# Kernel tuning notes

Measured on AMD Instinct MI355X. Metric: run time of the kernel, lower is better.

The kernel has to match this reference:

```python
import jax, jax.numpy as jnp
import numpy as np

EPS = 1e-8
N, C, R = 512, 32, 32


def _eijk():
    e = np.zeros((3, 3, 3), np.float32)
    e[0, 1, 2] = e[1, 2, 0] = e[2, 0, 1] = 1.0
    e[0, 2, 1] = e[2, 1, 0] = e[1, 0, 2] = -1.0
    return jnp.asarray(e)


def _unit(v):
    # unit_vectors: v / (|v| + EPS)
    return v / (jnp.linalg.norm(v, axis=-1, keepdims=True) + EPS)


def _y2(r):
    # real l=2 spherical harmonics (TFN convention), [N,N,5]
    x, y, z = r[..., 0], r[..., 1], r[..., 2]
    r2 = jnp.maximum(jnp.sum(r * r, axis=-1), EPS)
    c = float(2.0 * np.sqrt(3.0))
    return jnp.stack([
        x * y / r2,
        y * z / r2,
        (-x * x - y * y + 2.0 * z * z) / (c * r2),
        z * x / r2,
        (x * x - y * y) / (2.0 * r2),
    ], axis=-1)


def _forward(in0, in1, in2, rbf, rij,
             w1_f00, b1_f00, w2_f00, b2_f00,
             w1_f01, b1_f01, w2_f01, b2_f01,
             w1_f02, b1_f02, w2_f02, b2_f02,
             w1_f10, b1_f10, w2_f10, b2_f10,
             w1_f11, b1_f11, w2_f11, b2_f11):
    def rad(w1, b1, w2, b2):
        # RadialFunction: relu(b1 + rbf @ w1^T) @ w2^T + b2 -> [N,N,C]
        h = jax.nn.relu(b1 + jnp.einsum('abr,hr->abh', rbf, w1))
        return b2 + jnp.einsum('abh,ch->abc', h, w2)

    # mask self/zero-distance pairs (dij < EPS -> radial = 0), as in F_1/F_2
    mask = (jnp.linalg.norm(rij, axis=-1) >= EPS).astype(rbf.dtype)[..., None]  # [N,N,1]
    u = _unit(rij)    # [N,N,3]
    y2 = _y2(rij)     # [N,N,5]

    r00 = rad(w1_f00, b1_f00, w2_f00, b2_f00)            # scalar filter F_0
    r01 = rad(w1_f01, b1_f01, w2_f01, b2_f01) * mask     # F_1 radial, 0x1->1
    r02 = rad(w1_f02, b1_f02, w2_f02, b2_f02) * mask     # F_2 radial, 0x2->2
    r10 = rad(w1_f10, b1_f10, w2_f10, b2_f10) * mask     # F_1 radial, 1x1->0
    r11 = rad(w1_f11, b1_f11, w2_f11, b2_f11) * mask     # F_1 radial, 1x1->1

    # Filter_0_output_0 (identity CG): L x 0 -> L, aggregate over neighbors b
    o0_s = jnp.einsum('abf,bfi->afi', r00, in0)          # [N,C,1]
    o1_s = jnp.einsum('abf,bfi->afi', r00, in1)          # [N,C,3]
    o2_s = jnp.einsum('abf,bfi->afi', r00, in2)          # [N,C,5]
    o1_a = jnp.einsum('abi,abf,bf->afi', u, r01, in0[..., 0])
    o2_a = jnp.einsum('abi,abf,bf->afi', y2, r02, in0[..., 0])
    o0_b = jnp.einsum('abj,abf,bfj->af', u, r10, in1)[..., None]
    o1_c = jnp.einsum('ijk,abj,abf,bfk->afi', _eijk(), u, r11, in1)

    return (jnp.stack([o0_s, o0_b]),          # [2,N,C,1]
            jnp.stack([o1_a, o1_s, o1_c]),    # [3,N,C,3]
            jnp.stack([o2_a, o2_s]))          # [2,N,C,5]


def setup_inputs() -> dict:
    key = jax.random.key(0)
    ks = jax.random.split(key, 16)

    def xav(k, shape):
        lim = float(np.sqrt(6.0 / (shape[0] + shape[1])))
        return jax.random.uniform(k, shape, jnp.float32, -lim, lim)

    pos = jax.random.normal(ks[0], (N, 3), jnp.float32) * 3.0
    rij = pos[:, None, :] - pos[None, :, :]  # [N,N,3]; zero diagonal exercises the dij<EPS mask
    inp = {
        'in0': jax.random.normal(ks[1], (N, C, 1), jnp.float32),
        'in1': jax.random.normal(ks[2], (N, C, 3), jnp.float32),
        'in2': jax.random.normal(ks[3], (N, C, 5), jnp.float32),
        'rbf': jax.random.uniform(ks[4], (N, N, R), jnp.float32),
        'rij': rij,
    }
    for i, n in enumerate(['f00', 'f01', 'f02', 'f10', 'f11']):
        inp['w1_' + n] = xav(ks[5 + 2 * i], (R, R))
        inp['b1_' + n] = jnp.zeros((R,), jnp.float32)
        inp['w2_' + n] = xav(ks[6 + 2 * i], (C, R))
        inp['b2_' + n] = jnp.zeros((C,), jnp.float32)
    return inp


def reference(in0, in1, in2, rbf, rij,
              w1_f00, b1_f00, w2_f00, b2_f00,
              w1_f01, b1_f01, w2_f01, b2_f01,
              w1_f02, b1_f02, w2_f02, b2_f02,
              w1_f10, b1_f10, w2_f10, b2_f10,
              w1_f11, b1_f11, w2_f11, b2_f11):
    return _forward(in0, in1, in2, rbf, rij,
                    w1_f00, b1_f00, w2_f00, b2_f00,
                    w1_f01, b1_f01, w2_f01, b2_f01,
                    w1_f02, b1_f02, w2_f02, b2_f02,
                    w1_f10, b1_f10, w2_f10, b2_f10,
                    w1_f11, b1_f11, w2_f11, b2_f11)
```

## Files before the change

kernel.cpp:

```cpp
#include <hip/hip_runtime.h>
#include <math.h>

#define NN 512
#define CC 32
#define EPSF 1e-8f
#define WS 40

typedef __attribute__((ext_vector_type(8))) short bf16x8;
typedef __attribute__((ext_vector_type(4))) float f32x4;

__device__ __forceinline__ short f2bf(float f) {
    unsigned u = __float_as_uint(f);
    u += 0x7fffu + ((u >> 16) & 1u);
    return (short)(u >> 16);
}

#define STAGE_F(F, W1P, W2P)                                                   \
    {                                                                          \
        const int n0 = tid >> 5, k0 = tid & 31;                                \
        wlds[(((F) * 2 + 0) * 32 + n0) * WS + k0]      = f2bf((W1P)[tid]);     \
        wlds[(((F) * 2 + 0) * 32 + n0 + 16) * WS + k0] = f2bf((W1P)[tid+512]); \
        wlds[(((F) * 2 + 1) * 32 + n0) * WS + k0]      = f2bf((W2P)[tid]);     \
        wlds[(((F) * 2 + 1) * 32 + n0 + 16) * WS + k0] = f2bf((W2P)[tid+512]); \
    }

#define MLP3(WOFF, B1L, B1H, B2V, R)                                               \
    {                                                                              \
        const bf16x8 w1loM = *(const bf16x8*)&wlds[(WOFF) + ln * WS + q * 8];      \
        const bf16x8 w1hiM = *(const bf16x8*)&wlds[(WOFF) + (16 + ln) * WS + q * 8]; \
        f32x4 d0M = { (B1L), (B1L), (B1L), (B1L) };                                \
        f32x4 d1M = { (B1H), (B1H), (B1H), (B1H) };                                \
        d0M = __builtin_amdgcn_mfma_f32_16x16x32_bf16(rbfF, w1loM, d0M, 0, 0, 0);  \
        d1M = __builtin_amdgcn_mfma_f32_16x16x32_bf16(rbfF, w1hiM, d1M, 0, 0, 0);  \
        hlds[w][(q * 4 + 0) * WS + ln]      = f2bf(fmaxf(d0M[0], 0.f));            \
        hlds[w][(q * 4 + 1) * WS + ln]      = f2bf(fmaxf(d0M[1], 0.f));            \
        hlds[w][(q * 4 + 2) * WS + ln]      = f2bf(fmaxf(d0M[2], 0.f));            \
        hlds[w][(q * 4 + 3) * WS + ln]      = f2bf(fmaxf(d0M[3], 0.f));            \
        hlds[w][(q * 4 + 0) * WS + 16 + ln] = f2bf(fmaxf(d1M[0], 0.f));            \
        hlds[w][(q * 4 + 1) * WS + 16 + ln] = f2bf(fmaxf(d1M[1], 0.f));            \
        hlds[w][(q * 4 + 2) * WS + 16 + ln] = f2bf(fmaxf(d1M[2], 0.f));            \
        hlds[w][(q * 4 + 3) * WS + 16 + ln] = f2bf(fmaxf(d1M[3], 0.f));            \
        const bf16x8 hFM = *(const bf16x8*)&hlds[w][ln * WS + q * 8];              \
        const bf16x8 w2M = *(const bf16x8*)&wlds[(WOFF) + (32 + ch0 + ln) * WS + q * 8]; \
        f32x4 eM = { (B2V), (B2V), (B2V), (B2V) };                                 \
        R = __builtin_amdgcn_mfma_f32_16x16x32_bf16(hFM, w2M, eM, 0, 0, 0);        \
    }

#define AGGM(RR)                                                               \
    {                                                                          \
        const int bA = b0 + q * 4 + (RR);                                      \
        const f32x4 gA = *(const f32x4*)&geomall[bA][0];                       \
        const f32x4 gB = *(const f32x4*)&geomall[bA][4];                       \
        const float i0A = in0[bA * CC + cw];                                   \
        const float* i1A = in1 + (bA * CC + cw) * 3;                           \
        const float x1A = i1A[0], y1A = i1A[1], z1A = i1A[2];                  \
        const float* i2A = in2 + (bA * CC + cw) * 5;                           \
        const float p0A = i2A[0], p1A = i2A[1], p2A = i2A[2];                  \
        const float p3A = i2A[3], p4A = i2A[4];                                \
        const float s0A = rF0[(RR)];                                           \
        a0  = fmaf(s0A, i0A, a0);                                              \
        a5  = fmaf(s0A, x1A, a5);                                              \
        a6  = fmaf(s0A, y1A, a6);                                              \
        a7  = fmaf(s0A, z1A, a7);                                              \
        a16 = fmaf(s0A, p0A, a16);                                             \
        a17 = fmaf(s0A, p1A, a17);                                             \
        a18 = fmaf(s0A, p2A, a18);                                             \
        a19 = fmaf(s0A, p3A, a19);                                             \
        a20 = fmaf(s0A, p4A, a20);                                             \
        const float t1A = rF1[(RR)] * i0A;                                     \
        a2  = fmaf(t1A, gA[0], a2);                                            \
        a3  = fmaf(t1A, gA[1], a3);                                            \
        a4  = fmaf(t1A, gA[2], a4);                                            \
        const float t2A = rF2[(RR)] * i0A;                                     \
        a11 = fmaf(t2A, gA[3], a11);                                           \
        a12 = fmaf(t2A, gB[0], a12);                                           \
        a13 = fmaf(t2A, gB[1], a13);                                           \
        a14 = fmaf(t2A, gB[2], a14);                                           \
        a15 = fmaf(t2A, gB[3], a15);                                           \
        const float dtA = fmaf(gA[2], z1A, fmaf(gA[1], y1A, gA[0] * x1A));     \
        a1  = fmaf(rF3[(RR)], dtA, a1);                                        \
        const float cxA = fmaf(gA[1], z1A, -(gA[2] * y1A));                    \
        const float cyA = fmaf(gA[2], x1A, -(gA[0] * z1A));                    \
        const float czA = fmaf(gA[0], y1A, -(gA[1] * x1A));                    \
        a8  = fmaf(rF4[(RR)], cxA, a8);                                        \
        a9  = fmaf(rF4[(RR)], cyA, a9);                                        \
        a10 = fmaf(rF4[(RR)], czA, a10);                                       \
    }

#define RED(CMP, V)                                                            \
    {                                                                          \
        float vR = (V);                                                        \
        vR += __shfl_down(vR, 32);                                             \
        vR += __shfl_down(vR, 16);                                             \
        if (lane < 16) red[(w * 21 + (CMP)) * 16 + ln] = vR;                   \
    }

__global__ __launch_bounds__(512, 2) void tfn_mfma(
    const float* __restrict__ in0,
    const float* __restrict__ in1,
    const float* __restrict__ in2,
    const float* __restrict__ rbf,
    const float* __restrict__ rij,
    const float* __restrict__ w1_0, const float* __restrict__ b1_0,
    const float* __restrict__ w2_0, const float* __restrict__ b2_0,
    const float* __restrict__ w1_1, const float* __restrict__ b1_1,
    const float* __restrict__ w2_1, const float* __restrict__ b2_1,
    const float* __restrict__ w1_2, const float* __restrict__ b1_2,
    const float* __restrict__ w2_2, const float* __restrict__ b2_2,
    const float* __restrict__ w1_3, const float* __restrict__ b1_3,
    const float* __restrict__ w2_3, const float* __restrict__ b2_3,
    const float* __restrict__ w1_4, const float* __restrict__ b1_4,
    const float* __restrict__ w2_4, const float* __restrict__ b2_4,
    float* __restrict__ out)
{
    const int a    = blockIdx.x;
    const int tid  = threadIdx.x;
    const int w    = tid >> 6;
    const int lane = tid & 63;
    const int q    = lane >> 4;
    const int ln   = lane & 15;
    const int ch0  = (w & 1) * 16;
    const int cw   = ch0 + ln;

    __shared__ short wlds[5 * 2 * 32 * WS];
    __shared__ short hlds[8][16 * WS];
    __shared__ float geomall[NN][8];

    STAGE_F(0, w1_0, w2_0)
    STAGE_F(1, w1_1, w2_1)
    STAGE_F(2, w1_2, w2_2)
    STAGE_F(3, w1_3, w2_3)
    STAGE_F(4, w1_4, w2_4)

    const size_t rowbase = (size_t)a * NN;
    const float Y2C = 0.28867513459481287f;

    {
        const float* rp = rij + (rowbase + tid) * 3;
        const float x = rp[0], y = rp[1], z = rp[2];
        const float d2 = x * x + y * y + z * z;
        const float d  = sqrtf(d2);
        const float m  = (d >= EPSF) ? 1.f : 0.f;
        const float inv = m / (d + EPSF);
        const float ir2 = m / fmaxf(d2, EPSF);
        f32x4 gA = { x * inv, y * inv, z * inv, x * y * ir2 };
        f32x4 gB = { y * z * ir2, (2.f * z * z - x * x - y * y) * (ir2 * Y2C),
                     z * x * ir2, (x * x - y * y) * (ir2 * 0.5f) };
        *(f32x4*)&geomall[tid][0] = gA;
        *(f32x4*)&geomall[tid][4] = gB;
    }

    const float b1lo0 = b1_0[ln], b1hi0 = b1_0[16 + ln], b2v0 = b2_0[cw];
    const float b1lo1 = b1_1[ln], b1hi1 = b1_1[16 + ln], b2v1 = b2_1[cw];
    const float b1lo2 = b1_2[ln], b1hi2 = b1_2[16 + ln], b2v2 = b2_2[cw];
    const float b1lo3 = b1_3[ln], b1hi3 = b1_3[16 + ln], b2v3 = b2_3[cw];
    const float b1lo4 = b1_4[ln], b1hi4 = b1_4[16 + ln], b2v4 = b2_4[cw];
    __syncthreads();

    float a0 = 0.f, a1 = 0.f, a2 = 0.f, a3 = 0.f, a4 = 0.f, a5 = 0.f, a6 = 0.f;
    float a7 = 0.f, a8 = 0.f, a9 = 0.f, a10 = 0.f, a11 = 0.f, a12 = 0.f, a13 = 0.f;
    float a14 = 0.f, a15 = 0.f, a16 = 0.f, a17 = 0.f, a18 = 0.f, a19 = 0.f, a20 = 0.f;

    const int pairb = (w >> 1) * 128;

    const float* rbase = rbf + (rowbase + pairb + ln) * 32 + q * 8;
    f32x4 curA = *(const f32x4*)rbase;
    f32x4 curB = *(const f32x4*)(rbase + 4);

    #pragma unroll 1
    for (int t = 0; t < 8; ++t) {
        const int b0 = pairb + t * 16;

        bf16x8 rbfF;
        rbfF[0] = f2bf(curA[0]); rbfF[1] = f2bf(curA[1]);
        rbfF[2] = f2bf(curA[2]); rbfF[3] = f2bf(curA[3]);
        rbfF[4] = f2bf(curB[0]); rbfF[5] = f2bf(curB[1]);
        rbfF[6] = f2bf(curB[2]); rbfF[7] = f2bf(curB[3]);
        if (t < 7) {
            curA = *(const f32x4*)(rbase + (t + 1) * 512);
            curB = *(const f32x4*)(rbase + (t + 1) * 512 + 4);
        }

        f32x4 rF0, rF1, rF2, rF3, rF4;
        MLP3(0 * 64 * WS, b1lo0, b1hi0, b2v0, rF0)
        MLP3(1 * 64 * WS, b1lo1, b1hi1, b2v1, rF1)
        MLP3(2 * 64 * WS, b1lo2, b1hi2, b2v2, rF2)
        MLP3(3 * 64 * WS, b1lo3, b1hi3, b2v3, rF3)
        MLP3(4 * 64 * WS, b1lo4, b1hi4, b2v4, rF4)

        AGGM(0) AGGM(1) AGGM(2) AGGM(3)

        __builtin_amdgcn_sched_barrier(0);
    }

    __syncthreads();
    float* red = (float*)wlds;
    RED(0,  a0)  RED(1,  a1)  RED(2,  a2)  RED(3,  a3)  RED(4,  a4)
    RED(5,  a5)  RED(6,  a6)  RED(7,  a7)  RED(8,  a8)  RED(9,  a9)
    RED(10, a10) RED(11, a11) RED(12, a12) RED(13, a13) RED(14, a14)
    RED(15, a15) RED(16, a16) RED(17, a17) RED(18, a18) RED(19, a19)
    RED(20, a20)
    __syncthreads();

    const int NC = NN * CC;
    for (int e = tid; e < 21 * 32; e += 512) {
        const int cmp = e >> 5, c = e & 31;
        const int hh = c >> 4, l2 = c & 15;
        float s = 0.f;
        #pragma unroll
        for (int p = 0; p < 4; ++p)
            s += red[((p * 2 + hh) * 21 + cmp) * 16 + l2];
        int idx;
        if (cmp == 0)       idx = a * CC + c;
        else if (cmp == 1)  idx = NC + a * CC + c;
        else if (cmp < 5)   idx = 2 * NC + (a * CC + c) * 3 + (cmp - 2);
        else if (cmp < 8)   idx = 2 * NC + 3 * NC + (a * CC + c) * 3 + (cmp - 5);
        else if (cmp < 11)  idx = 2 * NC + 6 * NC + (a * CC + c) * 3 + (cmp - 8);
        else if (cmp < 16)  idx = 11 * NC + (a * CC + c) * 5 + (cmp - 11);
        else                idx = 11 * NC + 5 * NC + (a * CC + c) * 5 + (cmp - 16);
        out[idx] = s;
    }
}

extern "C" void kernel_launch(void* const* d_in, const int* in_sizes, int n_in,
                              void* d_out, int out_size, void* d_ws, size_t ws_size,
                              hipStream_t stream) {
    const float* in0 = (const float*)d_in[0];
    const float* in1 = (const float*)d_in[1];
    const float* in2 = (const float*)d_in[2];
    const float* rbf = (const float*)d_in[3];
    const float* rij = (const float*)d_in[4];

    hipLaunchKernelGGL(tfn_mfma, dim3(NN), dim3(512), 0, stream,
                       in0, in1, in2, rbf, rij,
                       (const float*)d_in[5],  (const float*)d_in[6],
                       (const float*)d_in[7],  (const float*)d_in[8],
                       (const float*)d_in[9],  (const float*)d_in[10],
                       (const float*)d_in[11], (const float*)d_in[12],
                       (const float*)d_in[13], (const float*)d_in[14],
                       (const float*)d_in[15], (const float*)d_in[16],
                       (const float*)d_in[17], (const float*)d_in[18],
                       (const float*)d_in[19], (const float*)d_in[20],
                       (const float*)d_in[21], (const float*)d_in[22],
                       (const float*)d_in[23], (const float*)d_in[24],
                       (float*)d_out);
}
```

Before: 42.09 us.

## Keep hidden MLP activations in registers via transposed MFMA and permuted W2 layout

The first-layer MFMA now has its operands swapped, so its transposed output lands in the lane layout the second MFMA needs as its A operand. This removes the per-filter round trip through the hidden LDS buffer. W2 is staged into LDS with a permuted k index so the K ordering matches the packed registers, and the b1 biases are loaded as per-lane vectors. The fp32-to-bf16 conversion uses the packed hardware instruction v_cvt_pk_bf16_f32 instead of manual rounding, which may round differently from the software path.

```diff
diff --git a/kernel.cpp b/kernel.cpp
--- a/kernel.cpp
+++ b/kernel.cpp
@@ -15,35 +15,36 @@
     return (short)(u >> 16);
 }
 
+__device__ __forceinline__ unsigned cvtpk(float lo, float hi) {
+    unsigned r;
+    asm("v_cvt_pk_bf16_f32 %0, %1, %2" : "=v"(r) : "v"(lo), "v"(hi));
+    return r;
+}
+
 #define STAGE_F(F, W1P, W2P)                                                   \
     {                                                                          \
-        const int n0 = tid >> 5, k0 = tid & 31;                                \
         wlds[(((F) * 2 + 0) * 32 + n0) * WS + k0]      = f2bf((W1P)[tid]);     \
         wlds[(((F) * 2 + 0) * 32 + n0 + 16) * WS + k0] = f2bf((W1P)[tid+512]); \
-        wlds[(((F) * 2 + 1) * 32 + n0) * WS + k0]      = f2bf((W2P)[tid]);     \
-        wlds[(((F) * 2 + 1) * 32 + n0 + 16) * WS + k0] = f2bf((W2P)[tid+512]); \
-    }
-
-#define MLP3(WOFF, B1L, B1H, B2V, R)                                               \
+        wlds[(((F) * 2 + 1) * 32 + n0) * WS + k2]      = f2bf((W2P)[tid]);     \
+        wlds[(((F) * 2 + 1) * 32 + n0 + 16) * WS + k2] = f2bf((W2P)[tid+512]); \
+    }
+
+#define MLP3S(WOFF, B1LO, B1HI, B2V, R)                                            \
     {                                                                              \
         const bf16x8 w1loM = *(const bf16x8*)&wlds[(WOFF) + ln * WS + q * 8];      \
         const bf16x8 w1hiM = *(const bf16x8*)&wlds[(WOFF) + (16 + ln) * WS + q * 8]; \
-        f32x4 d0M = { (B1L), (B1L), (B1L), (B1L) };                                \
-        f32x4 d1M = { (B1H), (B1H), (B1H), (B1H) };                                \
-        d0M = __builtin_amdgcn_mfma_f32_16x16x32_bf16(rbfF, w1loM, d0M, 0, 0, 0);  \
-        d1M = __builtin_amdgcn_mfma_f32_16x16x32_bf16(rbfF, w1hiM, d1M, 0, 0, 0);  \
-        hlds[w][(q * 4 + 0) * WS + ln]      = f2bf(fmaxf(d0M[0], 0.f));            \
-        hlds[w][(q * 4 + 1) * WS + ln]      = f2bf(fmaxf(d0M[1], 0.f));            \
-        hlds[w][(q * 4 + 2) * WS + ln]      = f2bf(fmaxf(d0M[2], 0.f));            \
-        hlds[w][(q * 4 + 3) * WS + ln]      = f2bf(fmaxf(d0M[3], 0.f));            \
-        hlds[w][(q * 4 + 0) * WS + 16 + ln] = f2bf(fmaxf(d1M[0], 0.f));            \
-        hlds[w][(q * 4 + 1) * WS + 16 + ln] = f2bf(fmaxf(d1M[1], 0.f));            \
-        hlds[w][(q * 4 + 2) * WS + 16 + ln] = f2bf(fmaxf(d1M[2], 0.f));            \
-        hlds[w][(q * 4 + 3) * WS + 16 + ln] = f2bf(fmaxf(d1M[3], 0.f));            \
-        const bf16x8 hFM = *(const bf16x8*)&hlds[w][ln * WS + q * 8];              \
+        f32x4 d0M = (B1LO);                                                        \
+        f32x4 d1M = (B1HI);                                                        \
+        d0M = __builtin_amdgcn_mfma_f32_16x16x32_bf16(w1loM, rbfF, d0M, 0, 0, 0);  \
+        d1M = __builtin_amdgcn_mfma_f32_16x16x32_bf16(w1hiM, rbfF, d1M, 0, 0, 0);  \
+        union { bf16x8 v; unsigned u[4]; } hu;                                     \
+        hu.u[0] = cvtpk(fmaxf(d0M[0], 0.f), fmaxf(d0M[1], 0.f));                   \
+        hu.u[1] = cvtpk(fmaxf(d0M[2], 0.f), fmaxf(d0M[3], 0.f));                   \
+        hu.u[2] = cvtpk(fmaxf(d1M[0], 0.f), fmaxf(d1M[1], 0.f));                   \
+        hu.u[3] = cvtpk(fmaxf(d1M[2], 0.f), fmaxf(d1M[3], 0.f));                   \
         const bf16x8 w2M = *(const bf16x8*)&wlds[(WOFF) + (32 + ch0 + ln) * WS + q * 8]; \
         f32x4 eM = { (B2V), (B2V), (B2V), (B2V) };                                 \
-        R = __builtin_amdgcn_mfma_f32_16x16x32_bf16(hFM, w2M, eM, 0, 0, 0);        \
+        R = __builtin_amdgcn_mfma_f32_16x16x32_bf16(hu.v, w2M, eM, 0, 0, 0);       \
     }
 
 #define AGGM(RR)                                                               \
@@ -123,8 +124,11 @@
     const int cw   = ch0 + ln;
 
     __shared__ short wlds[5 * 2 * 32 * WS];
-    __shared__ short hlds[8][16 * WS];
     __shared__ float geomall[NN][8];
+
+    const int n0 = tid >> 5, k0 = tid & 31;
+    const int k2 = (k0 < 16) ? ((k0 >> 2) * 8 + (k0 & 3))
+                             : (((k0 - 16) >> 2) * 8 + 4 + ((k0 - 16) & 3));
 
     STAGE_F(0, w1_0, w2_0)
     STAGE_F(1, w1_1, w2_1)
@@ -150,11 +154,13 @@
         *(f32x4*)&geomall[tid][4] = gB;
     }
 
-    const float b1lo0 = b1_0[ln], b1hi0 = b1_0[16 + ln], b2v0 = b2_0[cw];
-    const float b1lo1 = b1_1[ln], b1hi1 = b1_1[16 + ln], b2v1 = b2_1[cw];
-    const float b1lo2 = b1_2[ln], b1hi2 = b1_2[16 + ln], b2v2 = b2_2[cw];
-    const float b1lo3 = b1_3[ln], b1hi3 = b1_3[16 + ln], b2v3 = b2_3[cw];
-    const float b1lo4 = b1_4[ln], b1hi4 = b1_4[16 + ln], b2v4 = b2_4[cw];
+    const f32x4 b1lo0 = *(const f32x4*)(b1_0 + 4 * q), b1hi0 = *(const f32x4*)(b1_0 + 16 + 4 * q);
+    const f32x4 b1lo1 = *(const f32x4*)(b1_1 + 4 * q), b1hi1 = *(const f32x4*)(b1_1 + 16 + 4 * q);
+    const f32x4 b1lo2 = *(const f32x4*)(b1_2 + 4 * q), b1hi2 = *(const f32x4*)(b1_2 + 16 + 4 * q);
+    const f32x4 b1lo3 = *(const f32x4*)(b1_3 + 4 * q), b1hi3 = *(const f32x4*)(b1_3 + 16 + 4 * q);
+    const f32x4 b1lo4 = *(const f32x4*)(b1_4 + 4 * q), b1hi4 = *(const f32x4*)(b1_4 + 16 + 4 * q);
+    const float b2v0 = b2_0[cw], b2v1 = b2_1[cw], b2v2 = b2_2[cw];
+    const float b2v3 = b2_3[cw], b2v4 = b2_4[cw];
     __syncthreads();
 
     float a0 = 0.f, a1 = 0.f, a2 = 0.f, a3 = 0.f, a4 = 0.f, a5 = 0.f, a6 = 0.f;
@@ -171,22 +177,23 @@
     for (int t = 0; t < 8; ++t) {
         const int b0 = pairb + t * 16;
 
-        bf16x8 rbfF;
-        rbfF[0] = f2bf(curA[0]); rbfF[1] = f2bf(curA[1]);
-        rbfF[2] = f2bf(curA[2]); rbfF[3] = f2bf(curA[3]);
-        rbfF[4] = f2bf(curB[0]); rbfF[5] = f2bf(curB[1]);
-        rbfF[6] = f2bf(curB[2]); rbfF[7] = f2bf(curB[3]);
+        union { bf16x8 v; unsigned u[4]; } ru;
+        ru.u[0] = cvtpk(curA[0], curA[1]);
+        ru.u[1] = cvtpk(curA[2], curA[3]);
+        ru.u[2] = cvtpk(curB[0], curB[1]);
+        ru.u[3] = cvtpk(curB[2], curB[3]);
+        const bf16x8 rbfF = ru.v;
         if (t < 7) {
             curA = *(const f32x4*)(rbase + (t + 1) * 512);
             curB = *(const f32x4*)(rbase + (t + 1) * 512 + 4);
         }
 
         f32x4 rF0, rF1, rF2, rF3, rF4;
-        MLP3(0 * 64 * WS, b1lo0, b1hi0, b2v0, rF0)
-        MLP3(1 * 64 * WS, b1lo1, b1hi1, b2v1, rF1)
-        MLP3(2 * 64 * WS, b1lo2, b1hi2, b2v2, rF2)
-        MLP3(3 * 64 * WS, b1lo3, b1hi3, b2v3, rF3)
-        MLP3(4 * 64 * WS, b1lo4, b1hi4, b2v4, rF4)
+        MLP3S(0 * 64 * WS, b1lo0, b1hi0, b2v0, rF0)
+        MLP3S(1 * 64 * WS, b1lo1, b1hi1, b2v1, rF1)
+        MLP3S(2 * 64 * WS, b1lo2, b1hi2, b2v2, rF2)
+        MLP3S(3 * 64 * WS, b1lo3, b1hi3, b2v3, rF3)
+        MLP3S(4 * 64 * WS, b1lo4, b1hi4, b2v4, rF4)
 
         AGGM(0) AGGM(1) AGGM(2) AGGM(3)
 
```

Result: faster. 40.46 us (-3.9%).
